# Optimization experiments

Hardware: AMD Instinct MI355X
Metric: run time of the kernel (lower is better)

The kernel has to match this reference:

```python
import jax, jax.numpy as jnp
import numpy as np

TOP_K = 8
NUM_EXPERTS = 64


def setup_inputs() -> dict:
    key = jax.random.key(0)
    k1, k2 = jax.random.split(key)
    x = jax.random.normal(k1, (4, 4096, 2048), dtype=jnp.float32)
    # nn.Linear weight [num_experts, d_model], scaled like typical init
    gate_w = jax.random.normal(k2, (NUM_EXPERTS, 2048), dtype=jnp.float32) * 0.02
    expert_bias = jnp.zeros((NUM_EXPERTS,), dtype=jnp.float32)
    return {"x": x, "gate_w": gate_w, "expert_bias": expert_bias}


def reference(x, gate_w, expert_bias):
    # logits = gate(x): [b, s, E]
    logits = jnp.einsum("bsd,ed->bse", x, gate_w)
    # bias is detached in the original (routing-only, no grad)
    logits_with_bias = logits + jax.lax.stop_gradient(expert_bias)
    # top-k over experts
    top_k_logits, top_k_indices = jax.lax.top_k(logits_with_bias, TOP_K)
    # softmax over the small top-k dimension
    top_k_scores = jax.nn.softmax(top_k_logits, axis=-1)
    # scatter-add load counts per expert (training branch)
    flat_indices = top_k_indices.reshape(-1)
    expert_counts = jnp.zeros((NUM_EXPERTS,), dtype=jnp.int32).at[flat_indices].add(1)
    return top_k_scores, top_k_indices, expert_counts
```

## Files before the change

kernel.cpp:

```cpp
#include <hip/hip_runtime.h>
#include <math.h>

#define DIM   2048
#define NEXP  64
#define TOPK  8
#define ROWS  32
#define NT    512
#define NBLK  512

typedef __attribute__((ext_vector_type(8)))  short bf16x8;
typedef __attribute__((ext_vector_type(16))) float f32x16;

#define MFMA(A, B, C) __builtin_amdgcn_mfma_f32_32x32x16_bf16(A, B, C, 0, 0, 0)
#define AS_BF(v) (*(const bf16x8*)&(v))

typedef __attribute__((address_space(3))) unsigned int       lds_uint;
typedef __attribute__((address_space(1))) const unsigned int glb_uint;

#define STR2(x) #x
#define STR(x) STR2(x)
#define GL16(dst, p, off) \
    asm volatile("global_load_dwordx4 %0, %1, off offset:" STR(off) \
                 : "=v"(dst) : "v"(p) : "memory")

__device__ inline unsigned int bfpack(float a, float b) {
    unsigned int ua = __float_as_uint(a), ub = __float_as_uint(b);
    unsigned int lo = (ua + 0x7FFFu + ((ua >> 16) & 1u)) >> 16;
    unsigned int hi = (ub + 0x7FFFu + ((ub >> 16) & 1u)) & 0xFFFF0000u;
    return hi | lo;
}
__device__ inline void split2pair(float a, float b, unsigned int& h, unsigned int& m) {
    h = bfpack(a, b);
    float ra = a - __uint_as_float(h << 16);
    float rb = b - __uint_as_float(h & 0xFFFF0000u);
    m = bfpack(ra, rb);
}

__global__ __launch_bounds__(256) void prep_kernel(const float* __restrict__ w,
                                                   unsigned int* __restrict__ wpack) {
    const int u = blockIdx.x * 256 + threadIdx.x;
    const int e = u >> 8, k8 = u & 255;
    const float4 v0 = *(const float4*)(w + (size_t)e * DIM + k8 * 8);
    const float4 v1 = *(const float4*)(w + (size_t)e * DIM + k8 * 8 + 4);
    unsigned int h[4], m[4];
    split2pair(v0.x, v0.y, h[0], m[0]);
    split2pair(v0.z, v0.w, h[1], m[1]);
    split2pair(v1.x, v1.y, h[2], m[2]);
    split2pair(v1.z, v1.w, h[3], m[3]);
    const int wv = k8 >> 5, t = (k8 >> 1) & 15, kh = k8 & 1;
    const int eh = e >> 5, le = e & 31;
    char* base = (char*)wpack + (size_t)wv * 65536 + t * 4096
               + (eh * 2) * 1024 + (kh * 32 + le) * 16;
    *(uint4*)(base)        = (uint4){h[0], h[1], h[2], h[3]};
    *(uint4*)(base + 1024) = (uint4){m[0], m[1], m[2], m[3]};
}

__global__ __launch_bounds__(NT, 4) void router_kernel(
    const float* __restrict__ x,
    const unsigned int* __restrict__ wpack,
    const float* __restrict__ bias,
    float* __restrict__ out,
    int* __restrict__ histws,
    int M)
{
    __shared__ __align__(16) char smem[67584 + 256];

    const int tid  = threadIdx.x;
    const int bid  = blockIdx.x;
    const int swz  = (bid & 7) * (NBLK / 8) + (bid >> 3);
    const int row0 = swz * ROWS;
    int* hist = (int*)(smem + 67584);
    if (tid < NEXP) hist[tid] = 0;

    const int wv   = tid >> 6;
    const int lane = tid & 63;
    const int lr   = lane & 31;
    const int kh   = lane >> 5;

    const float* xg0 = x + (size_t)(row0 +  0 + (lane & 15)) * DIM + wv * 256 + (lane >> 4) * 4;
    const float* xg1 = x + (size_t)(row0 + 16 + (lane & 15)) * DIM + wv * 256 + (lane >> 4) * 4;
    const char* wsl = (const char*)wpack + (size_t)wv * 65536 + lane * 16;
    float* xtb = (float*)smem + wv * 1024;
    const int rdo = (lr >> 4) * 256 + kh * 128 + (lr & 15) * 4;

    f32x16 acc0 = {}, acc1 = {};
    uint4 wH0_0, wM0_0, wH1_0, wM1_0;
    uint4 wH0_1, wM0_1, wH1_1, wM1_1;

#define ISSUE(s, tt) do { \
        __builtin_amdgcn_global_load_lds((glb_uint*)(const void*)(xg0 + (tt) * 16), \
                                         (lds_uint*)(void*)(xtb + (s) * 512), 16, 0, 0); \
        __builtin_amdgcn_global_load_lds((glb_uint*)(const void*)(xg1 + (tt) * 16), \
                                         (lds_uint*)(void*)(xtb + (s) * 512 + 256), 16, 0, 0); \
        asm volatile("" ::: "memory"); \
        { const char* p_ = wsl + (tt) * 4096; \
          GL16(wH0_##s, p_, 0);    GL16(wM0_##s, p_, 1024); \
          GL16(wH1_##s, p_, 2048); GL16(wM1_##s, p_, 3072); } \
    } while (0)

#define DOSPLIT(vlo, vhi, hv, mv) do { \
        unsigned int h_[4], m_[4]; \
        split2pair((vlo).x, (vlo).y, h_[0], m_[0]); \
        split2pair((vlo).z, (vlo).w, h_[1], m_[1]); \
        split2pair((vhi).x, (vhi).y, h_[2], m_[2]); \
        split2pair((vhi).z, (vhi).w, h_[3], m_[3]); \
        hv = (uint4){h_[0], h_[1], h_[2], h_[3]}; \
        mv = (uint4){m_[0], m_[1], m_[2], m_[3]}; \
    } while (0)

#define KITER(s, WAITLIT, ISS) do { \
        asm volatile("s_waitcnt vmcnt(" WAITLIT ")" ::: "memory"); \
        __builtin_amdgcn_sched_barrier(0); \
        float4 alo_ = *(const float4*)(xtb + (s) * 512 + rdo); \
        float4 ahi_ = *(const float4*)(xtb + (s) * 512 + rdo + 64); \
        uint4 ah_, am_; \
        DOSPLIT(alo_, ahi_, ah_, am_); \
        acc0 = MFMA(AS_BF(ah_), AS_BF(wH0_##s), acc0); \
        acc0 = MFMA(AS_BF(am_), AS_BF(wH0_##s), acc0); \
        acc0 = MFMA(AS_BF(ah_), AS_BF(wM0_##s), acc0); \
        acc1 = MFMA(AS_BF(ah_), AS_BF(wH1_##s), acc1); \
        acc1 = MFMA(AS_BF(am_), AS_BF(wH1_##s), acc1); \
        acc1 = MFMA(AS_BF(ah_), AS_BF(wM1_##s), acc1); \
        __builtin_amdgcn_sched_barrier(0); \
        ISS; \
    } while (0)

    ISSUE(0, 0); ISSUE(1, 1);
    KITER(0, "6", ISSUE(0, 2));
    KITER(1, "6", ISSUE(1, 3));
    KITER(0, "6", ISSUE(0, 4));
    KITER(1, "6", ISSUE(1, 5));
    KITER(0, "6", ISSUE(0, 6));
    KITER(1, "6", ISSUE(1, 7));
    KITER(0, "6", ISSUE(0, 8));
    KITER(1, "6", ISSUE(1, 9));
    KITER(0, "6", ISSUE(0, 10));
    KITER(1, "6", ISSUE(1, 11));
    KITER(0, "6", ISSUE(0, 12));
    KITER(1, "6", ISSUE(1, 13));
    KITER(0, "6", ISSUE(0, 14));
    KITER(1, "6", ISSUE(1, 15));
    KITER(0, "6", );
    KITER(1, "0", );
#undef KITER
#undef DOSPLIT
#undef ISSUE

    __syncthreads();

    float* lgf = (float*)smem;
    #pragma unroll
    for (int r = 0; r < 16; ++r) {
        const int rr = (r & 3) + 8 * (r >> 2) + 4 * kh;
        lgf[(wv * 32 + rr) * 66 + lr]      = acc0[r];
        lgf[(wv * 32 + rr) * 66 + 32 + lr] = acc1[r];
    }
    __syncthreads();

    float* out_scores = out;
    float* out_idx    = out + (size_t)M * TOPK;

    #pragma unroll
    for (int i = 0; i < 4; ++i) {
        const int row = wv * 4 + i;
        float vm = bias[lane];
        #pragma unroll
        for (int p = 0; p < 8; ++p) vm += lgf[(p * 32 + row) * 66 + lane];

        float vals[TOPK];
        int   ids[TOPK];
        #pragma unroll
        for (int k = 0; k < TOPK; ++k) {
            float mv = vm;
            int   mi = lane;
            #pragma unroll
            for (int off = 32; off > 0; off >>= 1) {
                float ov = __shfl_xor(mv, off);
                int   oi = __shfl_xor(mi, off);
                if (ov > mv || (ov == mv && oi < mi)) { mv = ov; mi = oi; }
            }
            vals[k] = mv; ids[k] = mi;
            if (lane == mi) { vm = -INFINITY; atomicAdd(&hist[mi], 1); }
        }
        if (lane == 0) {
            const float m = vals[0];
            float e[TOPK];
            float ssum = 0.f;
            #pragma unroll
            for (int k = 0; k < TOPK; ++k) { e[k] = expf(vals[k] - m); ssum += e[k]; }
            const float inv = 1.0f / ssum;
            const size_t base = (size_t)(row0 + row) * TOPK;
            #pragma unroll
            for (int k = 0; k < TOPK; ++k) {
                out_scores[base + k] = e[k] * inv;
                out_idx[base + k]    = (float)ids[k];
            }
        }
    }

    __syncthreads();
    if (tid < NEXP) histws[bid * NEXP + tid] = hist[tid];
}

__global__ __launch_bounds__(512) void reduce_kernel(const int* __restrict__ histws,
                                                     float* __restrict__ counts) {
    __shared__ int part[8][NEXP];
    const int t = threadIdx.x;
    const int e = t & 63, c = t >> 6;
    int sm = 0;
    for (int b = c; b < NBLK; b += 8) sm += histws[b * NEXP + e];
    part[c][e] = sm;
    __syncthreads();
    if (t < NEXP) {
        int tot = 0;
        #pragma unroll
        for (int i = 0; i < 8; ++i) tot += part[i][t];
        counts[t] = (float)tot;
    }
}

extern "C" void kernel_launch(void* const* d_in, const int* in_sizes, int n_in,
                              void* d_out, int out_size, void* d_ws, size_t ws_size,
                              hipStream_t stream) {
    const float* x    = (const float*)d_in[0];
    const float* w    = (const float*)d_in[1];
    const float* bias = (const float*)d_in[2];
    float* out = (float*)d_out;
    const int M = in_sizes[0] / DIM;

    unsigned int* wpack = (unsigned int*)d_ws;
    int* histws = (int*)((char*)d_ws + (size_t)NEXP * DIM * 4);
    float* out_counts = out + (size_t)2 * M * TOPK;

    prep_kernel<<<64, 256, 0, stream>>>(w, wpack);
    router_kernel<<<NBLK, NT, 0, stream>>>(x, wpack, bias, out, histws, M);
    reduce_kernel<<<1, 512, 0, stream>>>(histws, out_counts);
}
```

Baseline: 71.70 us.

## Split fused router into GEMM kernel writing partials and separate top-k kernel

Splits the fused GEMM+top-k kernel in two. The GEMM kernel now writes per-wave split-K partial logits to global workspace instead of reducing them through LDS, and a new top-k kernel sums the 8 partials, adds the bias, selects the top-k and computes the softmax and histogram. This shrinks GEMM LDS use and may allow higher occupancy, but it adds an extra launch and about 8 MB of partial-logit global traffic.

```diff
diff --git a/kernel.cpp b/kernel.cpp
--- a/kernel.cpp
+++ b/kernel.cpp
@@ -55,22 +55,18 @@
     *(uint4*)(base + 1024) = (uint4){m[0], m[1], m[2], m[3]};
 }
 
-__global__ __launch_bounds__(NT, 4) void router_kernel(
+__global__ __launch_bounds__(NT) void gemm_kernel(
     const float* __restrict__ x,
     const unsigned int* __restrict__ wpack,
-    const float* __restrict__ bias,
-    float* __restrict__ out,
-    int* __restrict__ histws,
+    float* __restrict__ part,
     int M)
 {
-    __shared__ __align__(16) char smem[67584 + 256];
+    __shared__ __align__(16) float xtile[8192];
 
     const int tid  = threadIdx.x;
     const int bid  = blockIdx.x;
     const int swz  = (bid & 7) * (NBLK / 8) + (bid >> 3);
     const int row0 = swz * ROWS;
-    int* hist = (int*)(smem + 67584);
-    if (tid < NEXP) hist[tid] = 0;
 
     const int wv   = tid >> 6;
     const int lane = tid & 63;
@@ -80,7 +76,7 @@
     const float* xg0 = x + (size_t)(row0 +  0 + (lane & 15)) * DIM + wv * 256 + (lane >> 4) * 4;
     const float* xg1 = x + (size_t)(row0 + 16 + (lane & 15)) * DIM + wv * 256 + (lane >> 4) * 4;
     const char* wsl = (const char*)wpack + (size_t)wv * 65536 + lane * 16;
-    float* xtb = (float*)smem + wv * 1024;
+    float* xtb = xtile + wv * 1024;
     const int rdo = (lr >> 4) * 256 + kh * 128 + (lr & 15) * 4;
 
     f32x16 acc0 = {}, acc1 = {};
@@ -146,26 +142,37 @@
 #undef DOSPLIT
 #undef ISSUE
 
-    __syncthreads();
-
-    float* lgf = (float*)smem;
     #pragma unroll
     for (int r = 0; r < 16; ++r) {
         const int rr = (r & 3) + 8 * (r >> 2) + 4 * kh;
-        lgf[(wv * 32 + rr) * 66 + lr]      = acc0[r];
-        lgf[(wv * 32 + rr) * 66 + 32 + lr] = acc1[r];
+        float* p = part + ((size_t)wv * M + (row0 + rr)) * 64;
+        p[lr]      = acc0[r];
+        p[lr + 32] = acc1[r];
     }
+}
+
+__global__ __launch_bounds__(256) void topk_kernel(
+    const float* __restrict__ part,
+    const float* __restrict__ bias,
+    float* __restrict__ out,
+    int* __restrict__ histws,
+    int M)
+{
+    __shared__ int hist[NEXP];
+    const int tid = threadIdx.x, bid = blockIdx.x;
+    const int wv = tid >> 6, lane = tid & 63;
+    if (tid < NEXP) hist[tid] = 0;
     __syncthreads();
 
     float* out_scores = out;
     float* out_idx    = out + (size_t)M * TOPK;
-
-    #pragma unroll
-    for (int i = 0; i < 4; ++i) {
-        const int row = wv * 4 + i;
+    const int rbase = bid * 32 + wv * 8;
+
+    for (int i = 0; i < 8; ++i) {
+        const int row = rbase + i;
         float vm = bias[lane];
         #pragma unroll
-        for (int p = 0; p < 8; ++p) vm += lgf[(p * 32 + row) * 66 + lane];
+        for (int s = 0; s < 8; ++s) vm += part[((size_t)s * M + row) * 64 + lane];
 
         float vals[TOPK];
         int   ids[TOPK];
@@ -189,7 +196,7 @@
             #pragma unroll
             for (int k = 0; k < TOPK; ++k) { e[k] = expf(vals[k] - m); ssum += e[k]; }
             const float inv = 1.0f / ssum;
-            const size_t base = (size_t)(row0 + row) * TOPK;
+            const size_t base = (size_t)row * TOPK;
             #pragma unroll
             for (int k = 0; k < TOPK; ++k) {
                 out_scores[base + k] = e[k] * inv;
@@ -204,17 +211,17 @@
 
 __global__ __launch_bounds__(512) void reduce_kernel(const int* __restrict__ histws,
                                                      float* __restrict__ counts) {
-    __shared__ int part[8][NEXP];
+    __shared__ int partl[8][NEXP];
     const int t = threadIdx.x;
     const int e = t & 63, c = t >> 6;
     int sm = 0;
     for (int b = c; b < NBLK; b += 8) sm += histws[b * NEXP + e];
-    part[c][e] = sm;
+    partl[c][e] = sm;
     __syncthreads();
     if (t < NEXP) {
         int tot = 0;
         #pragma unroll
-        for (int i = 0; i < 8; ++i) tot += part[i][t];
+        for (int i = 0; i < 8; ++i) tot += partl[i][t];
         counts[t] = (float)tot;
     }
 }
@@ -229,10 +236,12 @@
     const int M = in_sizes[0] / DIM;
 
     unsigned int* wpack = (unsigned int*)d_ws;
-    int* histws = (int*)((char*)d_ws + (size_t)NEXP * DIM * 4);
+    int*   histws   = (int*)((char*)d_ws + (1u << 20));
+    float* partials = (float*)((char*)d_ws + (2u << 20));
     float* out_counts = out + (size_t)2 * M * TOPK;
 
     prep_kernel<<<64, 256, 0, stream>>>(w, wpack);
-    router_kernel<<<NBLK, NT, 0, stream>>>(x, wpack, bias, out, histws, M);
+    gemm_kernel<<<NBLK, NT, 0, stream>>>(x, wpack, partials, M);
+    topk_kernel<<<M / 32, 256, 0, stream>>>(partials, bias, out, histws, M);
     reduce_kernel<<<1, 512, 0, stream>>>(histws, out_counts);
 }
```

New measurement: 94.78 us. +32.2%, slower.

## Double rows per block to reuse weight fragments across two M tiles

Applied to the files above, without the earlier changes.

Each block now handles 64 rows instead of 32, so every loaded weight fragment (high and mid bf16 parts) feeds two row tiles' MFMAs. This halves the number of blocks and lowers the occupancy target from 4 to 2 blocks per CU. The cross-wave K reduction also changes: instead of writing all partials and summing at read time, waves accumulate serially into one LDS tile, with a barrier per wave. Total weight traffic drops, at the cost of more registers, fewer blocks in flight and eight serialized reduction steps.

```diff
diff --git a/kernel.cpp b/kernel.cpp
--- a/kernel.cpp
+++ b/kernel.cpp
@@ -4,9 +4,9 @@
 #define DIM   2048
 #define NEXP  64
 #define TOPK  8
-#define ROWS  32
+#define BM    64
 #define NT    512
-#define NBLK  512
+#define NBLK  256
 
 typedef __attribute__((ext_vector_type(8)))  short bf16x8;
 typedef __attribute__((ext_vector_type(16))) float f32x16;
@@ -55,7 +55,7 @@
     *(uint4*)(base + 1024) = (uint4){m[0], m[1], m[2], m[3]};
 }
 
-__global__ __launch_bounds__(NT, 4) void router_kernel(
+__global__ __launch_bounds__(NT, 2) void router_kernel(
     const float* __restrict__ x,
     const unsigned int* __restrict__ wpack,
     const float* __restrict__ bias,
@@ -63,13 +63,13 @@
     int* __restrict__ histws,
     int M)
 {
-    __shared__ __align__(16) char smem[67584 + 256];
+    __shared__ __align__(16) float xtile[16384];
+    __shared__ int hist[NEXP];
 
     const int tid  = threadIdx.x;
     const int bid  = blockIdx.x;
     const int swz  = (bid & 7) * (NBLK / 8) + (bid >> 3);
-    const int row0 = swz * ROWS;
-    int* hist = (int*)(smem + 67584);
+    const int row0 = swz * BM;
     if (tid < NEXP) hist[tid] = 0;
 
     const int wv   = tid >> 6;
@@ -77,21 +77,28 @@
     const int lr   = lane & 31;
     const int kh   = lane >> 5;
 
-    const float* xg0 = x + (size_t)(row0 +  0 + (lane & 15)) * DIM + wv * 256 + (lane >> 4) * 4;
-    const float* xg1 = x + (size_t)(row0 + 16 + (lane & 15)) * DIM + wv * 256 + (lane >> 4) * 4;
+    const float* xg00 = x + (size_t)(row0 +  0 + (lane & 15)) * DIM + wv * 256 + (lane >> 4) * 4;
+    const float* xg01 = x + (size_t)(row0 + 16 + (lane & 15)) * DIM + wv * 256 + (lane >> 4) * 4;
+    const float* xg10 = x + (size_t)(row0 + 32 + (lane & 15)) * DIM + wv * 256 + (lane >> 4) * 4;
+    const float* xg11 = x + (size_t)(row0 + 48 + (lane & 15)) * DIM + wv * 256 + (lane >> 4) * 4;
     const char* wsl = (const char*)wpack + (size_t)wv * 65536 + lane * 16;
-    float* xtb = (float*)smem + wv * 1024;
+    float* xtb = xtile + wv * 2048;
     const int rdo = (lr >> 4) * 256 + kh * 128 + (lr & 15) * 4;
 
-    f32x16 acc0 = {}, acc1 = {};
+    f32x16 acc00 = {}, acc01 = {}, acc10 = {}, acc11 = {};
     uint4 wH0_0, wM0_0, wH1_0, wM1_0;
     uint4 wH0_1, wM0_1, wH1_1, wM1_1;
 
 #define ISSUE(s, tt) do { \
-        __builtin_amdgcn_global_load_lds((glb_uint*)(const void*)(xg0 + (tt) * 16), \
-                                         (lds_uint*)(void*)(xtb + (s) * 512), 16, 0, 0); \
-        __builtin_amdgcn_global_load_lds((glb_uint*)(const void*)(xg1 + (tt) * 16), \
-                                         (lds_uint*)(void*)(xtb + (s) * 512 + 256), 16, 0, 0); \
+        float* d_ = xtb + (s) * 1024; \
+        __builtin_amdgcn_global_load_lds((glb_uint*)(const void*)(xg00 + (tt) * 16), \
+                                         (lds_uint*)(void*)(d_), 16, 0, 0); \
+        __builtin_amdgcn_global_load_lds((glb_uint*)(const void*)(xg01 + (tt) * 16), \
+                                         (lds_uint*)(void*)(d_ + 256), 16, 0, 0); \
+        __builtin_amdgcn_global_load_lds((glb_uint*)(const void*)(xg10 + (tt) * 16), \
+                                         (lds_uint*)(void*)(d_ + 512), 16, 0, 0); \
+        __builtin_amdgcn_global_load_lds((glb_uint*)(const void*)(xg11 + (tt) * 16), \
+                                         (lds_uint*)(void*)(d_ + 768), 16, 0, 0); \
         asm volatile("" ::: "memory"); \
         { const char* p_ = wsl + (tt) * 4096; \
           GL16(wH0_##s, p_, 0);    GL16(wM0_##s, p_, 1024); \
@@ -111,36 +118,45 @@
 #define KITER(s, WAITLIT, ISS) do { \
         asm volatile("s_waitcnt vmcnt(" WAITLIT ")" ::: "memory"); \
         __builtin_amdgcn_sched_barrier(0); \
-        float4 alo_ = *(const float4*)(xtb + (s) * 512 + rdo); \
-        float4 ahi_ = *(const float4*)(xtb + (s) * 512 + rdo + 64); \
+        float4 alo0_ = *(const float4*)(xtb + (s) * 1024 + rdo); \
+        float4 ahi0_ = *(const float4*)(xtb + (s) * 1024 + rdo + 64); \
+        float4 alo1_ = *(const float4*)(xtb + (s) * 1024 + 512 + rdo); \
+        float4 ahi1_ = *(const float4*)(xtb + (s) * 1024 + 512 + rdo + 64); \
         uint4 ah_, am_; \
-        DOSPLIT(alo_, ahi_, ah_, am_); \
-        acc0 = MFMA(AS_BF(ah_), AS_BF(wH0_##s), acc0); \
-        acc0 = MFMA(AS_BF(am_), AS_BF(wH0_##s), acc0); \
-        acc0 = MFMA(AS_BF(ah_), AS_BF(wM0_##s), acc0); \
-        acc1 = MFMA(AS_BF(ah_), AS_BF(wH1_##s), acc1); \
-        acc1 = MFMA(AS_BF(am_), AS_BF(wH1_##s), acc1); \
-        acc1 = MFMA(AS_BF(ah_), AS_BF(wM1_##s), acc1); \
+        DOSPLIT(alo0_, ahi0_, ah_, am_); \
+        acc00 = MFMA(AS_BF(ah_), AS_BF(wH0_##s), acc00); \
+        acc00 = MFMA(AS_BF(am_), AS_BF(wH0_##s), acc00); \
+        acc00 = MFMA(AS_BF(ah_), AS_BF(wM0_##s), acc00); \
+        acc01 = MFMA(AS_BF(ah_), AS_BF(wH1_##s), acc01); \
+        acc01 = MFMA(AS_BF(am_), AS_BF(wH1_##s), acc01); \
+        acc01 = MFMA(AS_BF(ah_), AS_BF(wM1_##s), acc01); \
+        DOSPLIT(alo1_, ahi1_, ah_, am_); \
+        acc10 = MFMA(AS_BF(ah_), AS_BF(wH0_##s), acc10); \
+        acc10 = MFMA(AS_BF(am_), AS_BF(wH0_##s), acc10); \
+        acc10 = MFMA(AS_BF(ah_), AS_BF(wM0_##s), acc10); \
+        acc11 = MFMA(AS_BF(ah_), AS_BF(wH1_##s), acc11); \
+        acc11 = MFMA(AS_BF(am_), AS_BF(wH1_##s), acc11); \
+        acc11 = MFMA(AS_BF(ah_), AS_BF(wM1_##s), acc11); \
         __builtin_amdgcn_sched_barrier(0); \
         ISS; \
     } while (0)
 
     ISSUE(0, 0); ISSUE(1, 1);
-    KITER(0, "6", ISSUE(0, 2));
-    KITER(1, "6", ISSUE(1, 3));
-    KITER(0, "6", ISSUE(0, 4));
-    KITER(1, "6", ISSUE(1, 5));
-    KITER(0, "6", ISSUE(0, 6));
-    KITER(1, "6", ISSUE(1, 7));
-    KITER(0, "6", ISSUE(0, 8));
-    KITER(1, "6", ISSUE(1, 9));
-    KITER(0, "6", ISSUE(0, 10));
-    KITER(1, "6", ISSUE(1, 11));
-    KITER(0, "6", ISSUE(0, 12));
-    KITER(1, "6", ISSUE(1, 13));
-    KITER(0, "6", ISSUE(0, 14));
-    KITER(1, "6", ISSUE(1, 15));
-    KITER(0, "6", );
+    KITER(0, "8", ISSUE(0, 2));
+    KITER(1, "8", ISSUE(1, 3));
+    KITER(0, "8", ISSUE(0, 4));
+    KITER(1, "8", ISSUE(1, 5));
+    KITER(0, "8", ISSUE(0, 6));
+    KITER(1, "8", ISSUE(1, 7));
+    KITER(0, "8", ISSUE(0, 8));
+    KITER(1, "8", ISSUE(1, 9));
+    KITER(0, "8", ISSUE(0, 10));
+    KITER(1, "8", ISSUE(1, 11));
+    KITER(0, "8", ISSUE(0, 12));
+    KITER(1, "8", ISSUE(1, 13));
+    KITER(0, "8", ISSUE(0, 14));
+    KITER(1, "8", ISSUE(1, 15));
+    KITER(0, "8", );
     KITER(1, "0", );
 #undef KITER
 #undef DOSPLIT
@@ -148,25 +164,34 @@
 
     __syncthreads();
 
-    float* lgf = (float*)smem;
-    #pragma unroll
-    for (int r = 0; r < 16; ++r) {
-        const int rr = (r & 3) + 8 * (r >> 2) + 4 * kh;
-        lgf[(wv * 32 + rr) * 66 + lr]      = acc0[r];
-        lgf[(wv * 32 + rr) * 66 + 32 + lr] = acc1[r];
+    float* lg = xtile;
+    for (int p = 0; p < 8; ++p) {
+        if (wv == p) {
+            #pragma unroll
+            for (int r = 0; r < 16; ++r) {
+                const int rr = (r & 3) + 8 * (r >> 2) + 4 * kh;
+                if (p == 0) {
+                    lg[rr * 66 + lr]             = acc00[r];
+                    lg[rr * 66 + 32 + lr]        = acc01[r];
+                    lg[(32 + rr) * 66 + lr]      = acc10[r];
+                    lg[(32 + rr) * 66 + 32 + lr] = acc11[r];
+                } else {
+                    lg[rr * 66 + lr]             += acc00[r];
+                    lg[rr * 66 + 32 + lr]        += acc01[r];
+                    lg[(32 + rr) * 66 + lr]      += acc10[r];
+                    lg[(32 + rr) * 66 + 32 + lr] += acc11[r];
+                }
+            }
+        }
+        __syncthreads();
     }
-    __syncthreads();
 
     float* out_scores = out;
     float* out_idx    = out + (size_t)M * TOPK;
 
-    #pragma unroll
-    for (int i = 0; i < 4; ++i) {
-        const int row = wv * 4 + i;
-        float vm = bias[lane];
-        #pragma unroll
-        for (int p = 0; p < 8; ++p) vm += lgf[(p * 32 + row) * 66 + lane];
-
+    for (int r8 = 0; r8 < 8; ++r8) {
+        const int row = wv * 8 + r8;
+        float vm = lg[row * 66 + lane] + bias[lane];
         float vals[TOPK];
         int   ids[TOPK];
         #pragma unroll
@@ -204,17 +229,17 @@
 
 __global__ __launch_bounds__(512) void reduce_kernel(const int* __restrict__ histws,
                                                      float* __restrict__ counts) {
-    __shared__ int part[8][NEXP];
+    __shared__ int partl[8][NEXP];
     const int t = threadIdx.x;
     const int e = t & 63, c = t >> 6;
     int sm = 0;
     for (int b = c; b < NBLK; b += 8) sm += histws[b * NEXP + e];
-    part[c][e] = sm;
+    partl[c][e] = sm;
     __syncthreads();
     if (t < NEXP) {
         int tot = 0;
         #pragma unroll
-        for (int i = 0; i < 8; ++i) tot += part[i][t];
+        for (int i = 0; i < 8; ++i) tot += partl[i][t];
         counts[t] = (float)tot;
     }
 }
@@ -229,7 +254,7 @@
     const int M = in_sizes[0] / DIM;
 
     unsigned int* wpack = (unsigned int*)d_ws;
-    int* histws = (int*)((char*)d_ws + (size_t)NEXP * DIM * 4);
+    int* histws = (int*)((char*)d_ws + (1u << 20));
     float* out_counts = out + (size_t)2 * M * TOPK;
 
     prep_kernel<<<64, 256, 0, stream>>>(w, wpack);
```

Result: slower. 84.05 us (+17.2%).

## Restructure router K-loop into block-cooperative double-buffered LDS pipeline

Applied to the files above, without the earlier changes.

The router kernel's x loading changes from per-wave private LDS slices to a block-wide cooperative DMA that fills a shared double buffer, so each wave now computes two K sub-tiles per phase across 8 phases with a workgroup barrier between them. The weight loads are widened to match. The aim is to cut the number of wait points and move to coarser, more coalesced loads with deeper prefetch. The cost is s_barrier synchronisation each phase and more live weight registers. The histogram workspace offset also moves to a fixed 1 MiB.

```diff
diff --git a/kernel.cpp b/kernel.cpp
--- a/kernel.cpp
+++ b/kernel.cpp
@@ -4,7 +4,7 @@
 #define DIM   2048
 #define NEXP  64
 #define TOPK  8
-#define ROWS  32
+#define BM    32
 #define NT    512
 #define NBLK  512
 
@@ -64,12 +64,13 @@
     int M)
 {
     __shared__ __align__(16) char smem[67584 + 256];
+    float* smemf = (float*)smem;
+    int* hist = (int*)(smem + 67584);
 
     const int tid  = threadIdx.x;
     const int bid  = blockIdx.x;
     const int swz  = (bid & 7) * (NBLK / 8) + (bid >> 3);
-    const int row0 = swz * ROWS;
-    int* hist = (int*)(smem + 67584);
+    const int row0 = swz * BM;
     if (tid < NEXP) hist[tid] = 0;
 
     const int wv   = tid >> 6;
@@ -77,25 +78,38 @@
     const int lr   = lane & 31;
     const int kh   = lane >> 5;
 
-    const float* xg0 = x + (size_t)(row0 +  0 + (lane & 15)) * DIM + wv * 256 + (lane >> 4) * 4;
-    const float* xg1 = x + (size_t)(row0 + 16 + (lane & 15)) * DIM + wv * 256 + (lane >> 4) * 4;
-    const char* wsl = (const char*)wpack + (size_t)wv * 65536 + lane * 16;
-    float* xtb = (float*)smem + wv * 1024;
+    const int rg  = (tid >> 6) & 1, r15 = tid & 15;
+    const int c   = (tid >> 4) & 3;
+    const float* xbase = x + (size_t)(row0 + rg * 16 + r15) * DIM
+                       + (tid >> 7) * 16 + c * 4;
+    float* dbase = smemf + tid * 4;
+
+    const char* wbase = (const char*)wpack + (2 * wv) * 4096 + lane * 16;
+
     const int rdo = (lr >> 4) * 256 + kh * 128 + (lr & 15) * 4;
+    const int cbase = (2 * wv) * 512 + rdo;
 
     f32x16 acc0 = {}, acc1 = {};
-    uint4 wH0_0, wM0_0, wH1_0, wM1_0;
-    uint4 wH0_1, wM0_1, wH1_1, wM1_1;
-
-#define ISSUE(s, tt) do { \
-        __builtin_amdgcn_global_load_lds((glb_uint*)(const void*)(xg0 + (tt) * 16), \
-                                         (lds_uint*)(void*)(xtb + (s) * 512), 16, 0, 0); \
-        __builtin_amdgcn_global_load_lds((glb_uint*)(const void*)(xg1 + (tt) * 16), \
-                                         (lds_uint*)(void*)(xtb + (s) * 512 + 256), 16, 0, 0); \
+    uint4 w0h_A, w0m_A, w0H_A, w0M_A, w1h_A, w1m_A, w1H_A, w1M_A;
+    uint4 w0h_B, w0m_B, w0H_B, w0M_B, w1h_B, w1m_B, w1H_B, w1M_B;
+
+#define DMA4(BUFO, PH) do { \
+        const float* s_ = xbase + (PH) * 256; \
+        float* d_ = dbase + (BUFO); \
+        __builtin_amdgcn_global_load_lds((glb_uint*)(const void*)(s_),       (lds_uint*)(void*)(d_),        16, 0, 0); \
+        __builtin_amdgcn_global_load_lds((glb_uint*)(const void*)(s_ +  64), (lds_uint*)(void*)(d_ + 2048), 16, 0, 0); \
+        __builtin_amdgcn_global_load_lds((glb_uint*)(const void*)(s_ + 128), (lds_uint*)(void*)(d_ + 4096), 16, 0, 0); \
+        __builtin_amdgcn_global_load_lds((glb_uint*)(const void*)(s_ + 192), (lds_uint*)(void*)(d_ + 6144), 16, 0, 0); \
         asm volatile("" ::: "memory"); \
-        { const char* p_ = wsl + (tt) * 4096; \
-          GL16(wH0_##s, p_, 0);    GL16(wM0_##s, p_, 1024); \
-          GL16(wH1_##s, p_, 2048); GL16(wM1_##s, p_, 3072); } \
+    } while (0)
+
+#define WLD(S, PH) do { \
+        const char* a_ = wbase + (PH) * 65536; \
+        const char* b_ = a_ + 4096; \
+        GL16(w0h_##S, a_, 0);    GL16(w0m_##S, a_, 1024); \
+        GL16(w0H_##S, a_, 2048); GL16(w0M_##S, a_, 3072); \
+        GL16(w1h_##S, b_, 0);    GL16(w1m_##S, b_, 1024); \
+        GL16(w1H_##S, b_, 2048); GL16(w1M_##S, b_, 3072); \
     } while (0)
 
 #define DOSPLIT(vlo, vhi, hv, mv) do { \
@@ -108,47 +122,53 @@
         mv = (uint4){m_[0], m_[1], m_[2], m_[3]}; \
     } while (0)
 
-#define KITER(s, WAITLIT, ISS) do { \
-        asm volatile("s_waitcnt vmcnt(" WAITLIT ")" ::: "memory"); \
-        __builtin_amdgcn_sched_barrier(0); \
-        float4 alo_ = *(const float4*)(xtb + (s) * 512 + rdo); \
-        float4 ahi_ = *(const float4*)(xtb + (s) * 512 + rdo + 64); \
+#define COMPUTE(S, BUFO) do { \
+        const float* c0_ = smemf + (BUFO) + cbase; \
+        float4 alo0_ = *(const float4*)(c0_); \
+        float4 ahi0_ = *(const float4*)(c0_ + 64); \
+        float4 alo1_ = *(const float4*)(c0_ + 512); \
+        float4 ahi1_ = *(const float4*)(c0_ + 576); \
         uint4 ah_, am_; \
-        DOSPLIT(alo_, ahi_, ah_, am_); \
-        acc0 = MFMA(AS_BF(ah_), AS_BF(wH0_##s), acc0); \
-        acc0 = MFMA(AS_BF(am_), AS_BF(wH0_##s), acc0); \
-        acc0 = MFMA(AS_BF(ah_), AS_BF(wM0_##s), acc0); \
-        acc1 = MFMA(AS_BF(ah_), AS_BF(wH1_##s), acc1); \
-        acc1 = MFMA(AS_BF(am_), AS_BF(wH1_##s), acc1); \
-        acc1 = MFMA(AS_BF(ah_), AS_BF(wM1_##s), acc1); \
-        __builtin_amdgcn_sched_barrier(0); \
-        ISS; \
-    } while (0)
-
-    ISSUE(0, 0); ISSUE(1, 1);
-    KITER(0, "6", ISSUE(0, 2));
-    KITER(1, "6", ISSUE(1, 3));
-    KITER(0, "6", ISSUE(0, 4));
-    KITER(1, "6", ISSUE(1, 5));
-    KITER(0, "6", ISSUE(0, 6));
-    KITER(1, "6", ISSUE(1, 7));
-    KITER(0, "6", ISSUE(0, 8));
-    KITER(1, "6", ISSUE(1, 9));
-    KITER(0, "6", ISSUE(0, 10));
-    KITER(1, "6", ISSUE(1, 11));
-    KITER(0, "6", ISSUE(0, 12));
-    KITER(1, "6", ISSUE(1, 13));
-    KITER(0, "6", ISSUE(0, 14));
-    KITER(1, "6", ISSUE(1, 15));
-    KITER(0, "6", );
-    KITER(1, "0", );
-#undef KITER
+        DOSPLIT(alo0_, ahi0_, ah_, am_); \
+        acc0 = MFMA(AS_BF(ah_), AS_BF(w0h_##S), acc0); \
+        acc0 = MFMA(AS_BF(am_), AS_BF(w0h_##S), acc0); \
+        acc0 = MFMA(AS_BF(ah_), AS_BF(w0m_##S), acc0); \
+        acc1 = MFMA(AS_BF(ah_), AS_BF(w0H_##S), acc1); \
+        acc1 = MFMA(AS_BF(am_), AS_BF(w0H_##S), acc1); \
+        acc1 = MFMA(AS_BF(ah_), AS_BF(w0M_##S), acc1); \
+        DOSPLIT(alo1_, ahi1_, ah_, am_); \
+        acc0 = MFMA(AS_BF(ah_), AS_BF(w1h_##S), acc0); \
+        acc0 = MFMA(AS_BF(am_), AS_BF(w1h_##S), acc0); \
+        acc0 = MFMA(AS_BF(ah_), AS_BF(w1m_##S), acc0); \
+        acc1 = MFMA(AS_BF(ah_), AS_BF(w1H_##S), acc1); \
+        acc1 = MFMA(AS_BF(am_), AS_BF(w1H_##S), acc1); \
+        acc1 = MFMA(AS_BF(ah_), AS_BF(w1M_##S), acc1); \
+    } while (0)
+
+#define VMW(N) do { asm volatile("s_waitcnt vmcnt(" STR(N) ")" ::: "memory"); \
+                    __builtin_amdgcn_sched_barrier(0); } while (0)
+#define BAR __builtin_amdgcn_s_barrier()
+
+    DMA4(0, 0); WLD(A, 0);
+    VMW(8); BAR;
+    DMA4(8192, 1); WLD(B, 1); VMW(12); COMPUTE(A, 0);    VMW(8); BAR;
+    DMA4(0,    2); WLD(A, 2); VMW(12); COMPUTE(B, 8192); VMW(8); BAR;
+    DMA4(8192, 3); WLD(B, 3); VMW(12); COMPUTE(A, 0);    VMW(8); BAR;
+    DMA4(0,    4); WLD(A, 4); VMW(12); COMPUTE(B, 8192); VMW(8); BAR;
+    DMA4(8192, 5); WLD(B, 5); VMW(12); COMPUTE(A, 0);    VMW(8); BAR;
+    DMA4(0,    6); WLD(A, 6); VMW(12); COMPUTE(B, 8192); VMW(8); BAR;
+    DMA4(8192, 7); WLD(B, 7); VMW(12); COMPUTE(A, 0);    VMW(8); BAR;
+    VMW(0); COMPUTE(B, 8192);
+
+#undef VMW
+#undef COMPUTE
 #undef DOSPLIT
-#undef ISSUE
-
-    __syncthreads();
-
-    float* lgf = (float*)smem;
+#undef WLD
+#undef DMA4
+
+    __syncthreads();
+
+    float* lgf = smemf;
     #pragma unroll
     for (int r = 0; r < 16; ++r) {
         const int rr = (r & 3) + 8 * (r >> 2) + 4 * kh;
@@ -204,17 +224,17 @@
 
 __global__ __launch_bounds__(512) void reduce_kernel(const int* __restrict__ histws,
                                                      float* __restrict__ counts) {
-    __shared__ int part[8][NEXP];
+    __shared__ int partl[8][NEXP];
     const int t = threadIdx.x;
     const int e = t & 63, c = t >> 6;
     int sm = 0;
     for (int b = c; b < NBLK; b += 8) sm += histws[b * NEXP + e];
-    part[c][e] = sm;
+    partl[c][e] = sm;
     __syncthreads();
     if (t < NEXP) {
         int tot = 0;
         #pragma unroll
-        for (int i = 0; i < 8; ++i) tot += part[i][t];
+        for (int i = 0; i < 8; ++i) tot += partl[i][t];
         counts[t] = (float)tot;
     }
 }
@@ -229,7 +249,7 @@
     const int M = in_sizes[0] / DIM;
 
     unsigned int* wpack = (unsigned int*)d_ws;
-    int* histws = (int*)((char*)d_ws + (size_t)NEXP * DIM * 4);
+    int* histws = (int*)((char*)d_ws + (1u << 20));
     float* out_counts = out + (size_t)2 * M * TOPK;
 
     prep_kernel<<<64, 256, 0, stream>>>(w, wpack);
```

New measurement: 74.04 us. 1.03x slower.
